# Kernel optimization log

Measured on AMD Instinct MI355X. Metric: run time of the kernel, lower is better.

## Reference

```python
import jax, jax.numpy as jnp
import numpy as np

DIM, H, M = 1024, 8, 512
DH = DIM // H


def setup_inputs() -> dict:
    key = jax.random.key(0)
    k1, k2 = jax.random.split(key)
    z = jax.random.normal(k1, (8, 4096, DIM), dtype=jnp.float32)
    codebook = jax.random.normal(k2, (H, M, DH), dtype=jnp.float32) * 0.02
    return {"z": z, "codebook": codebook}


def reference(z, codebook):
    """Hard straight-through multi-head VQ quantisation.

    z:        [B, L, dim]
    codebook: [H, M, d_head]
    Returns (z_q [B,L,dim], indices [B,L,H], per_head_distances [B,L,H]).
    """
    B, L, _ = z.shape
    z_h = z.reshape(B, L, H, DH)                       # [B,L,H,dh]
    # squared-L2 distances, batched over all heads at once
    z_sq = jnp.sum(z_h * z_h, axis=-1, keepdims=True)  # [B,L,H,1]
    c_sq = jnp.sum(codebook * codebook, axis=-1)       # [H,M]
    cross = jnp.einsum('blhd,hmd->blhm', z_h, codebook)
    dists = jnp.maximum(z_sq + c_sq[None, None] - 2.0 * cross, 0.0)  # [B,L,H,M]
    idx = jnp.argmin(dists, axis=-1)                   # [B,L,H]
    min_d = jnp.take_along_axis(dists, idx[..., None], axis=-1)[..., 0]  # [B,L,H]
    # gather nearest codebook entry per head: codebook[h, idx[b,l,h]]
    e = codebook[jnp.arange(H)[None, None, :], idx]    # [B,L,H,dh]
    # straight-through: forward value = e, gradient = identity to z
    z_q_h = z_h + jax.lax.stop_gradient(e - z_h)
    z_q = z_q_h.reshape(B, L, DIM)
    return z_q, idx, min_d
```

## Files before the change

kernel.cpp:

```cpp
#include <hip/hip_runtime.h>
#include <cfloat>
#include <cstdint>

#define H_    8
#define DH_   128
#define M_    512
#define DIM_  1024
#define BL_   32768

#define BPOS    128
#define THREADS 512
#define NC      128
#define NCHUNK  (M_ / NC)
#define CAP     16
#define EPS     0.02f

typedef _Float16 half8 __attribute__((ext_vector_type(8)));
typedef float floatx4 __attribute__((ext_vector_type(4)));

#define WS_CB_BYTES (H_ * M_ * DH_ * 2)
#define WS_CSQ_OFF  WS_CB_BYTES

#define OFF_Z16  0
#define OFF_CB   (OFF_Z16 + 32768)
#define OFF_ZSQ  (OFF_CB + 32768)
#define OFF_CSQ  (OFF_ZSQ + 512)
#define OFF_CNT  (OFF_CSQ + 512)
#define OFF_CI   (OFF_CNT + 512)
#define LDS_TOTAL (OFF_CI + 8192)

extern __shared__ char smem[];

__device__ __forceinline__ int swz(int row, int g) { return (g ^ (row & 15)) << 4; }

__device__ __forceinline__ half8 cvt8(float4 a, float4 b) {
    half8 h;
    h[0]=(_Float16)a.x; h[1]=(_Float16)a.y; h[2]=(_Float16)a.z; h[3]=(_Float16)a.w;
    h[4]=(_Float16)b.x; h[5]=(_Float16)b.y; h[6]=(_Float16)b.z; h[7]=(_Float16)b.w;
    return h;
}

__device__ __forceinline__ float exact_d(const float* __restrict__ zr,
                                         const float* __restrict__ cr,
                                         float zsq)
{
    float cx0=0,cx1=0,cx2=0,cx3=0,cq0=0,cq1=0,cq2=0,cq3=0;
    #pragma unroll 8
    for (int k4 = 0; k4 < 32; ++k4) {
        float4 a = *(const float4*)(zr + k4 * 4);
        float4 b = *(const float4*)(cr + k4 * 4);
        cx0 = fmaf(a.x, b.x, cx0); cx1 = fmaf(a.y, b.y, cx1);
        cx2 = fmaf(a.z, b.z, cx2); cx3 = fmaf(a.w, b.w, cx3);
        cq0 = fmaf(b.x, b.x, cq0); cq1 = fmaf(b.y, b.y, cq1);
        cq2 = fmaf(b.z, b.z, cq2); cq3 = fmaf(b.w, b.w, cq3);
    }
    float cross = (cx0 + cx1) + (cx2 + cx3);
    float csqe  = (cq0 + cq1) + (cq2 + cq3);
    float d = (zsq + csqe) - 2.0f * cross;
    return fmaxf(d, 0.f);
}

__global__ __launch_bounds__(256) void prep_kernel(const float* __restrict__ cbk,
                                                   half8* __restrict__ cbw,
                                                   float* __restrict__ csqw)
{
    int t = blockIdx.x * 256 + threadIdx.x;
    int g = t & 15;
    int row = t >> 4;
    int gs = g ^ (row & 15);
    const float* src = cbk + (size_t)row * DH_ + gs * 8;
    float4 v0 = *(const float4*)src;
    float4 v1 = *(const float4*)(src + 4);
    cbw[row * 16 + g] = cvt8(v0, v1);

    if (g == 0) {
        const float* cr = cbk + (size_t)row * DH_;
        float ax=0.f, ay=0.f, az=0.f, aw=0.f;
        #pragma unroll
        for (int c4 = 0; c4 < 32; ++c4) {
            float4 v = *(const float4*)(cr + c4 * 4);
            ax = fmaf(v.x, v.x, ax); ay = fmaf(v.y, v.y, ay);
            az = fmaf(v.z, v.z, az); aw = fmaf(v.w, v.w, aw);
        }
        csqw[row] = (ax + ay) + (az + aw);
    }
}

__global__ __launch_bounds__(THREADS, 4) void vq_kernel(
    const float* __restrict__ z,
    const float* __restrict__ cbk,
    const char*  __restrict__ cbw,
    const float* __restrict__ csqw,
    float* __restrict__ out_zq,
    float* __restrict__ out_idx,
    float* __restrict__ out_mind)
{
    char*  z16  = smem + OFF_Z16;
    char*  cbB  = smem + OFF_CB;
    float* zsqS = (float*)(smem + OFF_ZSQ);
    float* csqS = (float*)(smem + OFF_CSQ);
    int*   cntS = (int*)(smem + OFF_CNT);
    int*   candI = (int*)(smem + OFF_CI);

    const int tid   = threadIdx.x;
    const int lane  = tid & 63;
    const int w     = tid >> 6;
    const int bx    = blockIdx.x;
    const int h     = bx & 7;
    const int posBase = (bx >> 3) * BPOS;

    const float* zBlk = z   + (size_t)posBase * DIM_ + h * DH_;
    const float* cbH  = cbk + (size_t)h * M_ * DH_;
    const char*  cbWH = cbw + (size_t)h * M_ * 256;
    const float* csqHw = csqw + h * M_;

    #pragma unroll
    for (int it = 0; it < 4; ++it) {
        int off = tid * 16 + it * 8192;
        __builtin_amdgcn_global_load_lds(
            (const __attribute__((address_space(1))) unsigned int*)(cbWH + off),
            (__attribute__((address_space(3))) unsigned int*)(cbB + off),
            16, 0, 0);
    }
    if (tid < 32) {
        int off = tid * 16;
        __builtin_amdgcn_global_load_lds(
            (const __attribute__((address_space(1))) unsigned int*)((const char*)csqHw + off),
            (__attribute__((address_space(3))) unsigned int*)((char*)csqS + off),
            16, 0, 0);
    }
    if (tid < BPOS) cntS[tid] = 0;

    if (tid < BPOS) {
        const float* zr = zBlk + (size_t)tid * DIM_;
        float ax=0.f, ay=0.f, az=0.f, aw=0.f;
        #pragma unroll
        for (int k = 0; k < 16; ++k) {
            float4 v0 = *(const float4*)(zr + k * 8);
            float4 v1 = *(const float4*)(zr + k * 8 + 4);
            ax = fmaf(v0.x, v0.x, ax); ay = fmaf(v0.y, v0.y, ay);
            az = fmaf(v0.z, v0.z, az); aw = fmaf(v0.w, v0.w, aw);
            ax = fmaf(v1.x, v1.x, ax); ay = fmaf(v1.y, v1.y, ay);
            az = fmaf(v1.z, v1.z, az); aw = fmaf(v1.w, v1.w, aw);
            *(half8*)(z16 + tid * 256 + swz(tid, k)) = cvt8(v0, v1);
        }
        zsqS[tid] = (ax + ay) + (az + aw);
    }
    __syncthreads();

    half8 afr[4];
    {
        int row = (w << 4) + (lane & 15);
        #pragma unroll
        for (int ks = 0; ks < 4; ++ks)
            afr[ks] = *(const half8*)(z16 + row * 256 + swz(row, ks * 4 + (lane >> 4)));
    }

    float rmin[4] = {FLT_MAX, FLT_MAX, FLT_MAX, FLT_MAX};

    #pragma unroll
    for (int ch = 0; ch < NCHUNK; ++ch) {
        const int mBase = ch * NC;

        floatx4 acc[8];
        #pragma unroll
        for (int nt = 0; nt < 8; ++nt) acc[nt] = (floatx4){0.f, 0.f, 0.f, 0.f};

        #pragma unroll
        for (int ks = 0; ks < 4; ++ks) {
            int g = ks * 4 + (lane >> 4);
            half8 bn[8];
            #pragma unroll
            for (int nt = 0; nt < 8; ++nt) {
                int crow = nt * 16 + (lane & 15);
                bn[nt] = *(const half8*)(cbB + crow * 256 + swz(crow, g));
            }
            #pragma unroll
            for (int nt = 0; nt < 8; ++nt)
                acc[nt] = __builtin_amdgcn_mfma_f32_16x16x32_f16(afr[ks], bn[nt], acc[nt], 0, 0, 0);
        }

        float cs[8];
        #pragma unroll
        for (int nt = 0; nt < 8; ++nt) cs[nt] = csqS[nt * 16 + (lane & 15)];
        const int colm = mBase + (lane & 15);

        #pragma unroll
        for (int r = 0; r < 4; ++r) {
            float v[8];
            #pragma unroll
            for (int nt = 0; nt < 8; ++nt) v[nt] = fmaf(-2.f, acc[nt][r], cs[nt]);
            float pm = fminf(fminf(fminf(v[0], v[1]), fminf(v[2], v[3])),
                             fminf(fminf(v[4], v[5]), fminf(v[6], v[7])));
            pm = fminf(pm, __shfl_xor(pm, 1, 16));
            pm = fminf(pm, __shfl_xor(pm, 2, 16));
            pm = fminf(pm, __shfl_xor(pm, 4, 16));
            pm = fminf(pm, __shfl_xor(pm, 8, 16));
            rmin[r] = fminf(rmin[r], pm);
            float thr = rmin[r] + EPS;
            int row = (w << 4) + (lane >> 4) * 4 + r;
            #pragma unroll
            for (int nt = 0; nt < 8; ++nt) {
                if (v[nt] <= thr) {
                    int slot = atomicAdd(&cntS[row], 1);
                    if (slot < CAP) candI[row * CAP + slot] = colm + nt * 16;
                }
            }
        }

        if (ch < NCHUNK - 1) {
            __syncthreads();
            const char* src = cbWH + (size_t)(mBase + NC) * 256;
            #pragma unroll
            for (int it = 0; it < 4; ++it) {
                int off = tid * 16 + it * 8192;
                __builtin_amdgcn_global_load_lds(
                    (const __attribute__((address_space(1))) unsigned int*)(src + off),
                    (__attribute__((address_space(3))) unsigned int*)(cbB + off),
                    16, 0, 0);
            }
            if (tid < 32) {
                int off = tid * 16;
                __builtin_amdgcn_global_load_lds(
                    (const __attribute__((address_space(1))) unsigned int*)((const char*)csqHw + (mBase + NC) * 4 + off),
                    (__attribute__((address_space(3))) unsigned int*)((char*)csqS + off),
                    16, 0, 0);
            }
            __syncthreads();
        }
    }

    int bi;
    {
        int row = tid >> 2, j = tid & 3;
        int cnt = cntS[row];
        float zsq = zsqS[row];
        const float* zr = zBlk + (size_t)row * DIM_;

        float bd = FLT_MAX; bi = 0x7fffffff;
        if (cnt > CAP) {
            for (int m = j; m < M_; m += 4) {
                float d = exact_d(zr, cbH + (size_t)m * DH_, zsq);
                if (d < bd || (d == bd && m < bi)) { bd = d; bi = m; }
            }
        } else {
            for (int c = j; c < cnt; c += 4) {
                int m = candI[row * CAP + c];
                float d = exact_d(zr, cbH + (size_t)m * DH_, zsq);
                if (d < bd || (d == bd && m < bi)) { bd = d; bi = m; }
            }
        }
        #pragma unroll
        for (int off = 1; off < 4; off <<= 1) {
            float od = __shfl_xor(bd, off, 4);
            int   oi = __shfl_xor(bi, off, 4);
            if (od < bd || (od == bd && oi < bi)) { bd = od; bi = oi; }
        }
        if (bi < 0 || bi >= M_) bi = 0;
        if (j == 0) {
            size_t gp = (size_t)(posBase + row) * H_ + h;
            out_idx[gp]  = (float)bi;
            out_mind[gp] = bd;
        }
    }

    #pragma unroll
    for (int it = 0; it < 8; ++it) {
        int rl2 = it * 2 + (lane >> 5);
        int c4  = lane & 31;
        int m = __shfl(bi, rl2 << 2, 64);
        float4 v = *(const float4*)(cbH + (size_t)m * DH_ + c4 * 4);
        *(float4*)(out_zq + (size_t)(posBase + (w << 4) + rl2) * DIM_ + h * DH_ + c4 * 4) = v;
    }
}

extern "C" void kernel_launch(void* const* d_in, const int* in_sizes, int n_in,
                              void* d_out, int out_size, void* d_ws, size_t ws_size,
                              hipStream_t stream) {
    const float* z   = (const float*)d_in[0];
    const float* cbk = (const float*)d_in[1];

    float* zq    = (float*)d_out;
    float* oidx  = zq + (size_t)BL_ * DIM_;
    float* omind = oidx + (size_t)BL_ * H_;

    half8* cbw  = (half8*)d_ws;
    float* csqw = (float*)((char*)d_ws + WS_CSQ_OFF);

    hipLaunchKernelGGL(prep_kernel, dim3(256), dim3(256), 0, stream,
                       cbk, cbw, csqw);

    hipFuncSetAttribute((const void*)vq_kernel,
                        hipFuncAttributeMaxDynamicSharedMemorySize, LDS_TOTAL);

    dim3 grid((BL_ / BPOS) * H_);
    dim3 block(THREADS);
    hipLaunchKernelGGL(vq_kernel, grid, block, LDS_TOTAL, stream,
                       z, cbk, (const char*)cbw, csqw, zq, oidx, omind);
}
```

Baseline: 153.8 us.

## Double-buffer codebook chunks in LDS and load z fragments directly

```diff
diff --git a/kernel.cpp b/kernel.cpp
--- a/kernel.cpp
+++ b/kernel.cpp
@@ -12,6 +12,7 @@
 #define THREADS 512
 #define NC      128
 #define NCHUNK  (M_ / NC)
+#define CBUF    32768
 #define CAP     16
 #define EPS     0.02f
 
@@ -21,11 +22,10 @@
 #define WS_CB_BYTES (H_ * M_ * DH_ * 2)
 #define WS_CSQ_OFF  WS_CB_BYTES
 
-#define OFF_Z16  0
-#define OFF_CB   (OFF_Z16 + 32768)
-#define OFF_ZSQ  (OFF_CB + 32768)
+#define OFF_CB   0
+#define OFF_ZSQ  65536
 #define OFF_CSQ  (OFF_ZSQ + 512)
-#define OFF_CNT  (OFF_CSQ + 512)
+#define OFF_CNT  (OFF_CSQ + 1024)
 #define OFF_CI   (OFF_CNT + 512)
 #define LDS_TOTAL (OFF_CI + 8192)
 
@@ -95,7 +95,6 @@
     float* __restrict__ out_idx,
     float* __restrict__ out_mind)
 {
-    char*  z16  = smem + OFF_Z16;
     char*  cbB  = smem + OFF_CB;
     float* zsqS = (float*)(smem + OFF_ZSQ);
     float* csqS = (float*)(smem + OFF_CSQ);
@@ -131,36 +130,59 @@
     }
     if (tid < BPOS) cntS[tid] = 0;
 
+    half8 afr[4];
+    {
+        int row = (w << 4) + (lane & 15);
+        const float* zr = zBlk + (size_t)row * DIM_;
+        #pragma unroll
+        for (int ks = 0; ks < 4; ++ks) {
+            int g = ks * 4 + (lane >> 4);
+            float4 v0 = *(const float4*)(zr + g * 8);
+            float4 v1 = *(const float4*)(zr + g * 8 + 4);
+            afr[ks] = cvt8(v0, v1);
+        }
+    }
+
     if (tid < BPOS) {
         const float* zr = zBlk + (size_t)tid * DIM_;
         float ax=0.f, ay=0.f, az=0.f, aw=0.f;
         #pragma unroll
-        for (int k = 0; k < 16; ++k) {
-            float4 v0 = *(const float4*)(zr + k * 8);
-            float4 v1 = *(const float4*)(zr + k * 8 + 4);
-            ax = fmaf(v0.x, v0.x, ax); ay = fmaf(v0.y, v0.y, ay);
-            az = fmaf(v0.z, v0.z, az); aw = fmaf(v0.w, v0.w, aw);
-            ax = fmaf(v1.x, v1.x, ax); ay = fmaf(v1.y, v1.y, ay);
-            az = fmaf(v1.z, v1.z, az); aw = fmaf(v1.w, v1.w, aw);
-            *(half8*)(z16 + tid * 256 + swz(tid, k)) = cvt8(v0, v1);
+        for (int c4 = 0; c4 < 32; ++c4) {
+            float4 v = *(const float4*)(zr + c4 * 4);
+            ax = fmaf(v.x, v.x, ax); ay = fmaf(v.y, v.y, ay);
+            az = fmaf(v.z, v.z, az); aw = fmaf(v.w, v.w, aw);
         }
         zsqS[tid] = (ax + ay) + (az + aw);
     }
     __syncthreads();
-
-    half8 afr[4];
-    {
-        int row = (w << 4) + (lane & 15);
-        #pragma unroll
-        for (int ks = 0; ks < 4; ++ks)
-            afr[ks] = *(const half8*)(z16 + row * 256 + swz(row, ks * 4 + (lane >> 4)));
-    }
 
     float rmin[4] = {FLT_MAX, FLT_MAX, FLT_MAX, FLT_MAX};
 
     #pragma unroll
     for (int ch = 0; ch < NCHUNK; ++ch) {
         const int mBase = ch * NC;
+        const char*  cb   = cbB + (ch & 1) * CBUF;
+        const float* csqC = csqS + (ch & 1) * 128;
+
+        if (ch < NCHUNK - 1) {
+            const char* src = cbWH + (size_t)(mBase + NC) * 256;
+            char* dst = cbB + ((ch + 1) & 1) * CBUF;
+            #pragma unroll
+            for (int it = 0; it < 4; ++it) {
+                int off = tid * 16 + it * 8192;
+                __builtin_amdgcn_global_load_lds(
+                    (const __attribute__((address_space(1))) unsigned int*)(src + off),
+                    (__attribute__((address_space(3))) unsigned int*)(dst + off),
+                    16, 0, 0);
+            }
+            if (tid < 32) {
+                int off = tid * 16;
+                __builtin_amdgcn_global_load_lds(
+                    (const __attribute__((address_space(1))) unsigned int*)((const char*)csqHw + (mBase + NC) * 4 + off),
+                    (__attribute__((address_space(3))) unsigned int*)((char*)csqS + ((ch + 1) & 1) * 512 + off),
+                    16, 0, 0);
+            }
+        }
 
         floatx4 acc[8];
         #pragma unroll
@@ -173,7 +195,7 @@
             #pragma unroll
             for (int nt = 0; nt < 8; ++nt) {
                 int crow = nt * 16 + (lane & 15);
-                bn[nt] = *(const half8*)(cbB + crow * 256 + swz(crow, g));
+                bn[nt] = *(const half8*)(cb + crow * 256 + swz(crow, g));
             }
             #pragma unroll
             for (int nt = 0; nt < 8; ++nt)
@@ -182,7 +204,7 @@
 
         float cs[8];
         #pragma unroll
-        for (int nt = 0; nt < 8; ++nt) cs[nt] = csqS[nt * 16 + (lane & 15)];
+        for (int nt = 0; nt < 8; ++nt) cs[nt] = csqC[nt * 16 + (lane & 15)];
         const int colm = mBase + (lane & 15);
 
         #pragma unroll
@@ -208,26 +230,8 @@
             }
         }
 
-        if (ch < NCHUNK - 1) {
+        if (ch < NCHUNK - 1)
             __syncthreads();
-            const char* src = cbWH + (size_t)(mBase + NC) * 256;
-            #pragma unroll
-            for (int it = 0; it < 4; ++it) {
-                int off = tid * 16 + it * 8192;
-                __builtin_amdgcn_global_load_lds(
-                    (const __attribute__((address_space(1))) unsigned int*)(src + off),
-                    (__attribute__((address_space(3))) unsigned int*)(cbB + off),
-                    16, 0, 0);
-            }
-            if (tid < 32) {
-                int off = tid * 16;
-                __builtin_amdgcn_global_load_lds(
-                    (const __attribute__((address_space(1))) unsigned int*)((const char*)csqHw + (mBase + NC) * 4 + off),
-                    (__attribute__((address_space(3))) unsigned int*)((char*)csqS + off),
-                    16, 0, 0);
-            }
-            __syncthreads();
-        }
     }
 
     int bi;
```

New measurement: 163.1 us. 6.0% more time.
